# Kernel optimization log

Hardware: AMD Instinct MI355X
Metric: run time of the kernel (lower is better)

Reference implementation:

```python
import jax, jax.numpy as jnp
import numpy as np

BN_EPS = 1e-5


def setup_inputs() -> dict:
    key = jax.random.key(0)
    ks = jax.random.split(key, 6)
    N, C, T, V = 64, 64, 300, 25
    num_A, O = 3, 64
    x = jax.random.normal(ks[0], (N, C, T, V), dtype=jnp.float32)
    A = jax.random.uniform(ks[1], (num_A, V, V), dtype=jnp.float32)
    # 1x1 conv weights per adjacency branch: W[a, o, c], bias b[a, o]
    W = jax.random.normal(ks[2], (num_A, O, C), dtype=jnp.float32) * (1.0 / np.sqrt(C))
    b = jax.random.normal(ks[3], (num_A, O), dtype=jnp.float32) * 0.01
    gamma = jnp.ones((O,), dtype=jnp.float32)
    beta = jnp.zeros((O,), dtype=jnp.float32)
    return {"x": x, "A": A, "W": W, "b": b, "gamma": gamma, "beta": beta}


def reference(x, A, W, b, gamma, beta):
    # x: [N, C, T, V]; A: [num_A, V, V]; W: [num_A, O, C]; b: [num_A, O]
    # For each branch a: xa = x @ A_a over the joint dim V, then a 1x1 conv
    # (channel mix W_a + bias b_a), accumulated over branches.
    z = jnp.einsum('nctv,avw->anctw', x, A)          # [num_A, N, C, T, V]
    y = jnp.einsum('anctw,aoc->notw', z, W)          # [N, O, T, V]
    y = y + jnp.sum(b, axis=0)[None, :, None, None]
    # BatchNorm2d (training mode: batch statistics over N, T, V per channel)
    mean = jnp.mean(y, axis=(0, 2, 3), keepdims=True)
    var = jnp.mean((y - mean) ** 2, axis=(0, 2, 3), keepdims=True)
    y = (y - mean) * jax.lax.rsqrt(var + BN_EPS)
    y = y * gamma[None, :, None, None] + beta[None, :, None, None]
    return jax.nn.relu(y)
```

## Files before the change

kernel.cpp:

```cpp
#include <hip/hip_runtime.h>


typedef __attribute__((ext_vector_type(8))) short short8;
typedef __attribute__((ext_vector_type(4))) float f32x4;

static __device__ __forceinline__ float bf2f(unsigned short u) {
    return __uint_as_float(((unsigned)u) << 16);
}
static __device__ __forceinline__ unsigned short f2bf(float f) {
    unsigned u = __float_as_uint(f);
    u += 0x7FFFu + ((u >> 16) & 1u);
    return (unsigned short)(u >> 16);
}
static __device__ __forceinline__ unsigned pack2bf(float a, float b) {
    return (unsigned)f2bf(a) | ((unsigned)f2bf(b) << 16);
}

#define MFMA16(a, b, c) __builtin_amdgcn_mfma_f32_16x16x32_bf16((a), (b), (c), 0, 0, 0)

#define ZSTRIDE 72
#define NSLOT   64

__global__ __launch_bounds__(256, 6)
void gcn_k1(const void* __restrict__ xg, const void* __restrict__ Ag,
            const void* __restrict__ Wg, const void* __restrict__ gammag,
            float* __restrict__ pslots, unsigned short* __restrict__ y_ws)
{
    const int tid  = threadIdx.x;
    const int wv   = tid >> 6;
    const int lane = tid & 63;
    const int n16  = lane & 15;
    const int kg   = lane >> 4;
    const int bx   = blockIdx.x;
    const int nb   = bx / 75;
    const int tile = bx - nb * 75;

    const bool isbf = (*(const unsigned*)gammag) == 0x3F803F80u;

    __shared__ __align__(16) char pool[16384];
    unsigned short* const xs2 = (unsigned short*)pool;
    unsigned short* const zsT = (unsigned short*)pool;
    __shared__ __align__(16) unsigned short AsT[3 * 32 * 32];
    __shared__ float red[128];

    if (tid < 128) red[tid] = 0.f;

    short8 wfrag[3][2];
    #pragma unroll
    for (int a = 0; a < 3; ++a)
        #pragma unroll
        for (int k2 = 0; k2 < 2; ++k2) {
            const int off = (a * 64 + wv * 16 + n16) * 64 + k2 * 32 + kg * 8;
            if (isbf) {
                wfrag[a][k2] = *(const short8*)((const unsigned short*)Wg + off);
            } else {
                const float* wp = (const float*)Wg + off;
                const float4 w0 = *(const float4*)wp;
                const float4 w1 = *(const float4*)(wp + 4);
                short8 f;
                f[0] = (short)f2bf(w0.x); f[1] = (short)f2bf(w0.y);
                f[2] = (short)f2bf(w0.z); f[3] = (short)f2bf(w0.w);
                f[4] = (short)f2bf(w1.x); f[5] = (short)f2bf(w1.y);
                f[6] = (short)f2bf(w1.z); f[7] = (short)f2bf(w1.w);
                wfrag[a][k2] = f;
            }
        }

    for (int s = tid; s < 3072; s += 256) {
        const int a = s >> 10, w = (s >> 5) & 31, v = s & 31;
        unsigned short val = 0;
        if (v < 25 && w < 25) {
            const int src = (a * 25 + v) * 25 + w;
            val = isbf ? ((const unsigned short*)Ag)[src] : f2bf(((const float*)Ag)[src]);
        }
        AsT[s] = val;
    }

    {
        #pragma unroll
        for (int vv = 25; vv < 32; ++vv) xs2[tid * 32 + vv] = 0;
    }
    if (isbf) {
        const unsigned* xp = (const unsigned*)xg;
        for (int p = tid; p < 3200; p += 256) {
            const int c = p / 50, pc = p - c * 50;
            const unsigned u = xp[(nb * 64 + c) * 3750 + tile * 50 + pc];
            const int r0 = pc * 2, r1 = r0 + 1;
            const int dt0 = r0 / 25, v0 = r0 - dt0 * 25;
            const int dt1 = r1 / 25, v1 = r1 - dt1 * 25;
            xs2[(dt0 * 64 + c) * 32 + v0] = (unsigned short)(u & 0xFFFFu);
            xs2[(dt1 * 64 + c) * 32 + v1] = (unsigned short)(u >> 16);
        }
    } else {
        const float2* xp = (const float2*)xg;
        for (int p = tid; p < 3200; p += 256) {
            const int c = p / 50, pc = p - c * 50;
            const float2 f = xp[(nb * 64 + c) * 3750 + tile * 50 + pc];
            const int r0 = pc * 2, r1 = r0 + 1;
            const int dt0 = r0 / 25, v0 = r0 - dt0 * 25;
            const int dt1 = r1 / 25, v1 = r1 - dt1 * 25;
            xs2[(dt0 * 64 + c) * 32 + v0] = f2bf(f.x);
            xs2[(dt1 * 64 + c) * 32 + v1] = f2bf(f.y);
        }
    }

    __syncthreads();

    short8 af[4];
    #pragma unroll
    for (int mt = 0; mt < 4; ++mt)
        af[mt] = *(const short8*)&xs2[(wv * 64 + mt * 16 + n16) * 32 + kg * 8];

    __syncthreads();

    for (int s = tid; s < 432; s += 256)
        ((unsigned*)(zsT + 100 * ZSTRIDE))[s] = 0;

    f32x4 acc[7];
    const f32x4 zero4 = (f32x4){0.f, 0.f, 0.f, 0.f};
    #pragma unroll
    for (int mt = 0; mt < 7; ++mt) acc[mt] = zero4;

    #pragma unroll
    for (int a = 0; a < 3; ++a) {
        const short8 bA0 = *(const short8*)&AsT[(a * 32 +      n16) * 32 + kg * 8];
        const short8 bA1 = *(const short8*)&AsT[(a * 32 + 16 + n16) * 32 + kg * 8];
        #pragma unroll
        for (int mt = 0; mt < 4; ++mt) {
            const f32x4 d0 = MFMA16(af[mt], bA0, zero4);
            const f32x4 d1 = MFMA16(af[mt], bA1, zero4);
            const int h = mt * 16 + kg * 4;
            *(uint2*)&zsT[(wv * 25 + n16) * ZSTRIDE + h] =
                make_uint2(pack2bf(d0[0], d0[1]), pack2bf(d0[2], d0[3]));
            if (n16 < 9)
                *(uint2*)&zsT[(wv * 25 + 16 + n16) * ZSTRIDE + h] =
                    make_uint2(pack2bf(d1[0], d1[1]), pack2bf(d1[2], d1[3]));
        }
        __syncthreads();

        #pragma unroll
        for (int mt = 0; mt < 7; ++mt) {
            #pragma unroll
            for (int k2 = 0; k2 < 2; ++k2) {
                const short8 bf = *(const short8*)&zsT[(mt * 16 + n16) * ZSTRIDE
                                                       + k2 * 32 + kg * 8];
                acc[mt] = MFMA16(wfrag[a][k2], bf, acc[mt]);
            }
        }
        if (a < 2) __syncthreads();
    }

    #pragma unroll
    for (int r = 0; r < 4; ++r) {
        const int o = 16 * wv + kg * 4 + r;
        const unsigned rowbase = (unsigned)(nb * 64 + o) * 7500u + (unsigned)tile * 100u;
        float s = 0.f, q = 0.f;
        #pragma unroll
        for (int mt = 0; mt < 7; ++mt) {
            const float v = acc[mt][r];
            const bool valid = (mt < 6) | (n16 < 4);
            const float vm = valid ? v : 0.f;
            s += vm; q += vm * vm;
            const float vhi = __shfl_xor(v, 1);
            if (((n16 & 1) == 0) && valid)
                *(unsigned*)(y_ws + rowbase + (unsigned)(mt * 16 + n16)) = pack2bf(v, vhi);
        }
        #pragma unroll
        for (int off = 1; off < 16; off <<= 1) {
            s += __shfl_xor(s, off);
            q += __shfl_xor(q, off);
        }
        if (n16 == 0) { atomicAdd(&red[o], s); atomicAdd(&red[64 + o], q); }
    }

    __syncthreads();
    if (tid < 128) atomicAdd(&pslots[(bx & (NSLOT - 1)) * 128 + tid], red[tid]);
}

__global__ __launch_bounds__(128)
void gcn_kred(const float* __restrict__ pslots, float* __restrict__ gfin)
{
    const int t = threadIdx.x;
    float s = 0.f;
    #pragma unroll
    for (int sl = 0; sl < NSLOT; ++sl)
        s += pslots[sl * 128 + t];
    gfin[t] = s;
}

__global__ __launch_bounds__(256)
void gcn_k2(const float* __restrict__ gfin, const unsigned* __restrict__ y32,
            const void* __restrict__ gammag, const void* __restrict__ betag,
            void* __restrict__ outg)
{
    __shared__ float sc[64], sh[64];
    const int tid = threadIdx.x;
    const bool isbf = (*(const unsigned*)gammag) == 0x3F803F80u;

    if (tid < 64) {
        const float inv  = 1.0f / 480000.0f;
        const float mean = gfin[tid] * inv;
        const float var  = gfin[64 + tid] * inv - mean * mean;
        const float rstd = rsqrtf(var + 1e-5f);
        float g, be;
        if (isbf) { g = bf2f(((const unsigned short*)gammag)[tid]); be = bf2f(((const unsigned short*)betag)[tid]); }
        else      { g = ((const float*)gammag)[tid];                be = ((const float*)betag)[tid]; }
        sc[tid] = g * rstd;
        sh[tid] = be - mean * g * rstd;
    }
    __syncthreads();

    const unsigned i = blockIdx.x * 256u + (unsigned)tid;
    const uint4 u = ((const uint4*)y32)[i];
    const unsigned b = i * 4u;
    unsigned wv[4] = {u.x, u.y, u.z, u.w};
    float res[8];
    #pragma unroll
    for (int j = 0; j < 4; ++j) {
        const unsigned o = ((b + j) / 3750u) & 63u;
        const float scl = sc[o], shf = sh[o];
        const float v0 = bf2f((unsigned short)(wv[j] & 0xFFFFu));
        const float v1 = bf2f((unsigned short)(wv[j] >> 16));
        res[2 * j]     = fmaxf(fmaf(v0, scl, shf), 0.f);
        res[2 * j + 1] = fmaxf(fmaf(v1, scl, shf), 0.f);
    }
    if (isbf) {
        uint4 outp;
        outp.x = (unsigned)f2bf(res[0]) | ((unsigned)f2bf(res[1]) << 16);
        outp.y = (unsigned)f2bf(res[2]) | ((unsigned)f2bf(res[3]) << 16);
        outp.z = (unsigned)f2bf(res[4]) | ((unsigned)f2bf(res[5]) << 16);
        outp.w = (unsigned)f2bf(res[6]) | ((unsigned)f2bf(res[7]) << 16);
        ((uint4*)outg)[i] = outp;
    } else {
        float4 f0 = make_float4(res[0], res[1], res[2], res[3]);
        float4 f1 = make_float4(res[4], res[5], res[6], res[7]);
        ((float4*)outg)[2 * i]     = f0;
        ((float4*)outg)[2 * i + 1] = f1;
    }
}

extern "C" void kernel_launch(void* const* d_in, const int* in_sizes, int n_in,
                              void* d_out, int out_size, void* d_ws, size_t ws_size,
                              hipStream_t stream)
{
    (void)in_sizes; (void)n_in; (void)out_size; (void)ws_size;
    const void* x     = d_in[0];
    const void* A     = d_in[1];
    const void* W     = d_in[2];
    const void* gamma = d_in[4];
    const void* beta  = d_in[5];

    float*          pslots = (float*)d_ws;
    float*          gfin   = (float*)((char*)d_ws + 32768);
    unsigned short* y_ws   = (unsigned short*)((char*)d_ws + 33280);

    hipMemsetAsync(d_ws, 0, 32768, stream);
    gcn_k1<<<dim3(64 * 75), dim3(256), 0, stream>>>(x, A, W, gamma, pslots, y_ws);
    gcn_kred<<<dim3(1), dim3(128), 0, stream>>>(pslots, gfin);
    gcn_k2<<<dim3(15000), dim3(256), 0, stream>>>(gfin, (const unsigned*)y_ws, gamma, beta, d_out);
}
```

Measured before the change: 327.0 us.

## Load x MFMA fragments directly from global memory, skipping LDS staging

The x tile is no longer staged through shared memory. Each lane now reads its 8-element bf16 MFMA A-fragment straight from global memory, overreading into the next time step where the K padding would be; those extra lanes are multiplied by zeroed rows of a relaid-out A matrix. This drops the LDS scatter writes, one barrier and the LDS read-back, at the cost of less coalesced global reads, unaligned handling on odd time steps, and a lower occupancy hint in launch bounds. The shared pool is replaced by a dedicated zsT buffer, and the bf16 packing helpers are tidied up.

```diff
diff --git a/kernel.cpp b/kernel.cpp
--- a/kernel.cpp
+++ b/kernel.cpp
@@ -20,8 +20,11 @@
 
 #define ZSTRIDE 72
 #define NSLOT   64
-
-__global__ __launch_bounds__(256, 6)
+#define XTOT    30720000u
+
+union U16x8 { uint4 q; unsigned u[4]; short8 s; unsigned short h[8]; };
+
+__global__ __launch_bounds__(256, 5)
 void gcn_k1(const void* __restrict__ xg, const void* __restrict__ Ag,
             const void* __restrict__ Wg, const void* __restrict__ gammag,
             float* __restrict__ pslots, unsigned short* __restrict__ y_ws)
@@ -34,16 +37,17 @@
     const int bx   = blockIdx.x;
     const int nb   = bx / 75;
     const int tile = bx - nb * 75;
+    const int t    = tile * 4 + wv;
 
     const bool isbf = (*(const unsigned*)gammag) == 0x3F803F80u;
 
-    __shared__ __align__(16) char pool[16384];
-    unsigned short* const xs2 = (unsigned short*)pool;
-    unsigned short* const zsT = (unsigned short*)pool;
-    __shared__ __align__(16) unsigned short AsT[3 * 32 * 32];
+    __shared__ __align__(16) unsigned short zsT[112 * ZSTRIDE];
+    __shared__ __align__(16) unsigned short AsT[3 * 4 * 32 * 8];
     __shared__ float red[128];
 
     if (tid < 128) red[tid] = 0.f;
+    for (int s = tid; s < 432; s += 256)
+        ((unsigned*)(zsT + 100 * ZSTRIDE))[s] = 0;
 
     short8 wfrag[3][2];
     #pragma unroll
@@ -57,12 +61,10 @@
                 const float* wp = (const float*)Wg + off;
                 const float4 w0 = *(const float4*)wp;
                 const float4 w1 = *(const float4*)(wp + 4);
-                short8 f;
-                f[0] = (short)f2bf(w0.x); f[1] = (short)f2bf(w0.y);
-                f[2] = (short)f2bf(w0.z); f[3] = (short)f2bf(w0.w);
-                f[4] = (short)f2bf(w1.x); f[5] = (short)f2bf(w1.y);
-                f[6] = (short)f2bf(w1.z); f[7] = (short)f2bf(w1.w);
-                wfrag[a][k2] = f;
+                U16x8 f;
+                f.u[0] = pack2bf(w0.x, w0.y); f.u[1] = pack2bf(w0.z, w0.w);
+                f.u[2] = pack2bf(w1.x, w1.y); f.u[3] = pack2bf(w1.z, w1.w);
+                wfrag[a][k2] = f.s;
             }
         }
 
@@ -73,48 +75,55 @@
             const int src = (a * 25 + v) * 25 + w;
             val = isbf ? ((const unsigned short*)Ag)[src] : f2bf(((const float*)Ag)[src]);
         }
-        AsT[s] = val;
-    }
-
-    {
-        #pragma unroll
-        for (int vv = 25; vv < 32; ++vv) xs2[tid * 32 + vv] = 0;
-    }
+        AsT[((a * 4 + (v >> 3)) * 32 + w) * 8 + (v & 7)] = val;
+    }
+
+    short8 af[4];
     if (isbf) {
-        const unsigned* xp = (const unsigned*)xg;
-        for (int p = tid; p < 3200; p += 256) {
-            const int c = p / 50, pc = p - c * 50;
-            const unsigned u = xp[(nb * 64 + c) * 3750 + tile * 50 + pc];
-            const int r0 = pc * 2, r1 = r0 + 1;
-            const int dt0 = r0 / 25, v0 = r0 - dt0 * 25;
-            const int dt1 = r1 / 25, v1 = r1 - dt1 * 25;
-            xs2[(dt0 * 64 + c) * 32 + v0] = (unsigned short)(u & 0xFFFFu);
-            xs2[(dt1 * 64 + c) * 32 + v1] = (unsigned short)(u >> 16);
+        const unsigned short* xb = (const unsigned short*)xg;
+        #pragma unroll
+        for (int mt = 0; mt < 4; ++mt) {
+            const unsigned base = ((unsigned)(nb * 64 + mt * 16 + n16) * 300u
+                                   + (unsigned)t) * 25u + (unsigned)(kg * 8);
+            U16x8 r;
+            if (base + 8u > XTOT) {
+                r.q = make_uint4(0, 0, 0, 0);
+                r.h[0] = xb[base];
+            } else if ((t & 1) == 0) {
+                const unsigned* p = (const unsigned*)(xb + base);
+                r.u[0] = p[0]; r.u[1] = p[1]; r.u[2] = p[2]; r.u[3] = p[3];
+            } else {
+                const unsigned* p = (const unsigned*)(xb + base - 1);
+                const unsigned tail = xb[base + 7];
+                r.u[0] = (p[0] >> 16) | (p[1] << 16);
+                r.u[1] = (p[1] >> 16) | (p[2] << 16);
+                r.u[2] = (p[2] >> 16) | (p[3] << 16);
+                r.u[3] = (p[3] >> 16) | (tail    << 16);
+            }
+            af[mt] = r.s;
         }
     } else {
-        const float2* xp = (const float2*)xg;
-        for (int p = tid; p < 3200; p += 256) {
-            const int c = p / 50, pc = p - c * 50;
-            const float2 f = xp[(nb * 64 + c) * 3750 + tile * 50 + pc];
-            const int r0 = pc * 2, r1 = r0 + 1;
-            const int dt0 = r0 / 25, v0 = r0 - dt0 * 25;
-            const int dt1 = r1 / 25, v1 = r1 - dt1 * 25;
-            xs2[(dt0 * 64 + c) * 32 + v0] = f2bf(f.x);
-            xs2[(dt1 * 64 + c) * 32 + v1] = f2bf(f.y);
+        const float* xf = (const float*)xg;
+        #pragma unroll
+        for (int mt = 0; mt < 4; ++mt) {
+            const unsigned base = ((unsigned)(nb * 64 + mt * 16 + n16) * 300u
+                                   + (unsigned)t) * 25u + (unsigned)(kg * 8);
+            U16x8 r;
+            if (base + 8u > XTOT) {
+                r.q = make_uint4(0, 0, 0, 0);
+                r.h[0] = f2bf(xf[base]);
+            } else {
+                float f[8];
+                #pragma unroll
+                for (int j = 0; j < 8; ++j) f[j] = xf[base + j];
+                r.u[0] = pack2bf(f[0], f[1]); r.u[1] = pack2bf(f[2], f[3]);
+                r.u[2] = pack2bf(f[4], f[5]); r.u[3] = pack2bf(f[6], f[7]);
+            }
+            af[mt] = r.s;
         }
     }
 
     __syncthreads();
-
-    short8 af[4];
-    #pragma unroll
-    for (int mt = 0; mt < 4; ++mt)
-        af[mt] = *(const short8*)&xs2[(wv * 64 + mt * 16 + n16) * 32 + kg * 8];
-
-    __syncthreads();
-
-    for (int s = tid; s < 432; s += 256)
-        ((unsigned*)(zsT + 100 * ZSTRIDE))[s] = 0;
 
     f32x4 acc[7];
     const f32x4 zero4 = (f32x4){0.f, 0.f, 0.f, 0.f};
@@ -123,8 +132,8 @@
 
     #pragma unroll
     for (int a = 0; a < 3; ++a) {
-        const short8 bA0 = *(const short8*)&AsT[(a * 32 +      n16) * 32 + kg * 8];
-        const short8 bA1 = *(const short8*)&AsT[(a * 32 + 16 + n16) * 32 + kg * 8];
+        const short8 bA0 = *(const short8*)&AsT[((a * 4 + kg) * 32 +      n16) * 8];
+        const short8 bA1 = *(const short8*)&AsT[((a * 4 + kg) * 32 + 16 + n16) * 8];
         #pragma unroll
         for (int mt = 0; mt < 4; ++mt) {
             const f32x4 d0 = MFMA16(af[mt], bA0, zero4);
@@ -226,10 +235,10 @@
     }
     if (isbf) {
         uint4 outp;
-        outp.x = (unsigned)f2bf(res[0]) | ((unsigned)f2bf(res[1]) << 16);
-        outp.y = (unsigned)f2bf(res[2]) | ((unsigned)f2bf(res[3]) << 16);
-        outp.z = (unsigned)f2bf(res[4]) | ((unsigned)f2bf(res[5]) << 16);
-        outp.w = (unsigned)f2bf(res[6]) | ((unsigned)f2bf(res[7]) << 16);
+        outp.x = pack2bf(res[0], res[1]);
+        outp.y = pack2bf(res[2], res[3]);
+        outp.z = pack2bf(res[4], res[5]);
+        outp.w = pack2bf(res[6], res[7]);
         ((uint4*)outg)[i] = outp;
     } else {
         float4 f0 = make_float4(res[0], res[1], res[2], res[3]);
```

New measurement: 332.9 us. Within noise of the previous version (+1.8%).
